# Performance work log

Hardware: AMD Instinct MI355X
Metric: run time of the kernel (lower is better)

## Reference

```python
import jax, jax.numpy as jnp
import numpy as np

B, L, K, NRBF = 2, 2048, 32, 16
NODE_F, EDGE_F = 128, 128
MAX_REL = 32  # af2 relpos -> 2*32+1 = 65 bins
NODE_IN, EDGE_IN = 21 + 6 + 8, 65 + 25 * NRBF + 1 + 2


def _ln(x, g, b, eps=1e-5):
    mu = jnp.mean(x, -1, keepdims=True)
    var = jnp.var(x, -1, keepdims=True)
    return (x - mu) / jnp.sqrt(var + eps) * g + b


def _normalize(t):
    return jnp.nan_to_num(t / jnp.linalg.norm(t, axis=-1, keepdims=True))


def _dihedral(p0, p1, p2, p3):
    u0, u1, u2 = p2 - p1, p0 - p1, p3 - p2
    n1 = _normalize(jnp.cross(u0, u1))
    n2 = _normalize(jnp.cross(u0, u2))
    sgn = jnp.sign(jnp.sum(jnp.cross(u1, u2) * u0, -1))
    return jnp.nan_to_num(sgn * jnp.arccos(jnp.sum(n1 * n2, -1)))


def setup_inputs() -> dict:
    key = jax.random.key(0)
    ks = jax.random.split(key, 9)
    return {
        "X": jax.random.normal(ks[0], (B, L, 4, 3), jnp.float32) * 5.0,
        "S": jax.random.randint(ks[1], (B, L), 0, 21),
        "BB_D_sincos": jax.random.normal(ks[2], (B, L, 3, 2), jnp.float32),
        "SC_D_sincos": jax.random.normal(ks[3], (B, L, 4, 2), jnp.float32),
        "chain_indices": jax.random.randint(ks[4], (B, L), 0, 2),
        "mask": jnp.ones((B, L), jnp.float32),
        "W_node": jax.random.normal(ks[5], (NODE_IN, NODE_F), jnp.float32) * 0.05,
        "b_node": jnp.zeros((NODE_F,), jnp.float32),
        "g_node": jnp.ones((NODE_F,), jnp.float32),
        "beta_node": jnp.zeros((NODE_F,), jnp.float32),
        "W_edge": jax.random.normal(ks[6], (EDGE_IN, EDGE_F), jnp.float32) * 0.05,
        "b_edge": jnp.zeros((EDGE_F,), jnp.float32),
        "g_edge": jnp.ones((EDGE_F,), jnp.float32),
        "beta_edge": jnp.zeros((EDGE_F,), jnp.float32),
    }


def reference(X, S, BB_D_sincos, SC_D_sincos, chain_indices, mask,
              W_node, b_node, g_node, beta_node,
              W_edge, b_edge, g_edge, beta_edge):
    Bn, Ln = X.shape[:2]
    N, Ca, C, O = X[:, :, 0], X[:, :, 1], X[:, :, 2], X[:, :, 3]
    # ---- masked pairwise Ca distances + kNN topk (smallest) ----
    m2 = mask[:, None, :] * mask[:, :, None]                      # [B,L,L]
    dX = Ca[:, :, None, :] - Ca[:, None, :, :]
    D = m2 * jnp.sqrt(jnp.sum(dX * dX, -1) + 1e-6)
    D_adj = D + 2.0 * (1.0 - m2) * jnp.max(D, -1, keepdims=True)
    _, E_idx = jax.lax.top_k(-D_adj, K)                           # [B,L,K]
    bidx = jnp.arange(Bn)[:, None, None]
    # ---- af2 relative-position one-hot (residue_index=None path) ----
    offset = E_idx - jnp.arange(Ln)[None, :, None]
    E_pos = jax.nn.one_hot(jnp.clip(offset + MAX_REL, 0, 2 * MAX_REL),
                           2 * MAX_REL + 1, dtype=jnp.float32)    # [B,L,K,65]
    # ---- impute CB, 5x5 atomic-distance RBFs at neighbors only ----
    bv, cv = Ca - N, C - Ca
    Cb = -0.58273431 * jnp.cross(bv, cv) + 0.56802827 * bv - 0.54067466 * cv + Ca
    X5 = jnp.stack((N, Ca, C, O, Cb), axis=-2)                    # [B,L,5,3]
    X5_nb = X5[bidx, E_idx]                                       # [B,L,K,5,3]
    dA = X5[:, :, None, :, None, :] - X5_nb[:, :, :, None, :, :]  # [B,L,K,5i,5j,3]
    Dn = jnp.sqrt(jnp.sum(dA * dA, -1) + 1e-6)                    # [B,L,K,5,5]
    mu = jnp.linspace(0.0, 20.0, NRBF)
    sigma = 20.0 / NRBF
    RBF_all = jnp.exp(-(((Dn[..., None] - mu) / sigma) ** 2))
    RBF_all = RBF_all.reshape(Bn, Ln, K, 25 * NRBF)               # i-major, j, rbf order
    # ---- edge type: same-chain indicator + 1 ----
    ch_nb = chain_indices[bidx, E_idx]
    E_type = ((ch_nb == chain_indices[:, :, None]).astype(jnp.float32) + 1.0)[..., None]
    # ---- pairwise dihedrals, evaluated only at neighbors ----
    N_nb, Ca_nb, C_nb = N[bidx, E_idx], Ca[bidx, E_idx], C[bidx, E_idx]
    ir_phi = _dihedral(C[:, :, None, :], N_nb, Ca_nb, C_nb)
    ir_psi = _dihedral(N[:, :, None, :], Ca[:, :, None, :], C[:, :, None, :], N_nb)
    dihed = jnp.stack((ir_phi, ir_psi), -1)                       # [B,L,K,2]
    # ---- fuse + embed ----
    E = jnp.concatenate((E_pos, RBF_all, E_type, dihed), -1)      # [B,L,K,468]
    V = jnp.concatenate((jax.nn.one_hot(S, 21, dtype=jnp.float32),
                         BB_D_sincos.reshape(Bn, Ln, -1),
                         SC_D_sincos.reshape(Bn, Ln, -1)), -1)    # [B,L,35]
    h_V = _ln(V @ W_node + b_node, g_node, beta_node)
    h_E = _ln(E @ W_edge + b_edge, g_edge, beta_edge)
    return (h_V, h_E, E_idx, X)
```

## Files before the change

kernel.cpp:

```cpp
#include <hip/hip_runtime.h>
#include <math.h>

#define NB 2
#define NL 2048
#define NK 32
#define NODE_F 128
#define EDGE_F 128

#define OFF_HV   0
#define OFF_HE   (NB*NL*NODE_F)
#define OFF_EIDX (OFF_HE + NB*NL*NK*EDGE_F)
#define OFF_X    (OFF_EIDX + NB*NL*NK)

#define ACH 7
#define BCH 6
#define SAW 232

typedef __attribute__((ext_vector_type(8))) short v8s;
typedef __attribute__((ext_vector_type(4))) float v4f;

__device__ __forceinline__ short f2bf(float f) {
    unsigned u = __float_as_uint(f);
    unsigned r = u + 0x7fffu + ((u >> 16) & 1u);
    return (short)(r >> 16);
}

#if __has_builtin(__builtin_amdgcn_exp2f)
#define EXP2F(x) __builtin_amdgcn_exp2f(x)
#else
#define EXP2F(x) __expf((x) * 0.6931471805599453f)
#endif

__device__ __forceinline__ unsigned bfpack(float f0, float f1) {
    unsigned u0 = __float_as_uint(f0), u1 = __float_as_uint(f1);
#if __has_builtin(__builtin_amdgcn_perm)
    return __builtin_amdgcn_perm(u1, u0, 0x07060302u);
#else
    return (u1 & 0xFFFF0000u) | (u0 >> 16);
#endif
}

template<int CTRL>
__device__ __forceinline__ unsigned long long dpp_min_step(unsigned long long x) {
    unsigned lo = (unsigned)x, hi = (unsigned)(x >> 32);
    unsigned plo = (unsigned)__builtin_amdgcn_update_dpp((int)lo, (int)lo, CTRL, 0xF, 0xF, false);
    unsigned phi = (unsigned)__builtin_amdgcn_update_dpp((int)hi, (int)hi, CTRL, 0xF, 0xF, false);
    unsigned long long p = (((unsigned long long)phi) << 32) | plo;
    return p < x ? p : x;
}
__device__ __forceinline__ unsigned long long wave_min_u64_dpp(unsigned long long x) {
    x = dpp_min_step<0xB1>(x);
    x = dpp_min_step<0x4E>(x);
    x = dpp_min_step<0x141>(x);
    x = dpp_min_step<0x140>(x);
    x = dpp_min_step<0x142>(x);
    x = dpp_min_step<0x143>(x);
    return x;
}

__device__ __forceinline__ void cross3(const float a[3], const float b[3], float c[3]) {
    c[0] = a[1]*b[2] - a[2]*b[1];
    c[1] = a[2]*b[0] - a[0]*b[2];
    c[2] = a[0]*b[1] - a[1]*b[0];
}
__device__ __forceinline__ float dot3(const float a[3], const float b[3]) {
    return a[0]*b[0] + a[1]*b[1] + a[2]*b[2];
}
__device__ float dihedral_f(const float p0[3], const float p1[3],
                            const float p2[3], const float p3[3]) {
    float u0[3], u1[3], u2[3];
    for (int d = 0; d < 3; d++) {
        u0[d] = p2[d] - p1[d];
        u1[d] = p0[d] - p1[d];
        u2[d] = p3[d] - p2[d];
    }
    float n1[3], n2[3], c12[3];
    cross3(u0, u1, n1);
    cross3(u0, u2, n2);
    cross3(u1, u2, c12);
    float l1 = sqrtf(dot3(n1, n1));
    float l2 = sqrtf(dot3(n2, n2));
    float cosang = dot3(n1, n2) / (l1 * l2);
    float s = dot3(c12, u0);
    float sgn = (s > 0.f) ? 1.f : ((s < 0.f) ? -1.f : 0.f);
    float r = sgn * acosf(cosang);
    return isnan(r) ? 0.f : r;
}

#define KNN_QMIN(Q) {                                                                  \
    unsigned long long a_ = key[(Q)*8+0] < key[(Q)*8+1] ? key[(Q)*8+0] : key[(Q)*8+1]; \
    unsigned long long b_ = key[(Q)*8+2] < key[(Q)*8+3] ? key[(Q)*8+2] : key[(Q)*8+3]; \
    unsigned long long c_ = key[(Q)*8+4] < key[(Q)*8+5] ? key[(Q)*8+4] : key[(Q)*8+5]; \
    unsigned long long d_ = key[(Q)*8+6] < key[(Q)*8+7] ? key[(Q)*8+6] : key[(Q)*8+7]; \
    a_ = a_ < b_ ? a_ : b_; c_ = c_ < d_ ? c_ : d_;                                    \
    qm[(Q)] = a_ < c_ ? a_ : c_; }

#define KNN_STEP(Q) {                                                                  \
    _Pragma("unroll")                                                                  \
    for (int i_ = 0; i_ < 8; i_++)                                                     \
        key[(Q)*8+i_] = (me && tstar == (Q)*8+i_) ? ~0ull : key[(Q)*8+i_];             \
    KNN_QMIN(Q) }

__global__ __launch_bounds__(256) void fused_pre_kernel(const float* __restrict__ X,
                                                        const float* __restrict__ mask,
                                                        const int* __restrict__ S,
                                                        const float* __restrict__ BB,
                                                        const float* __restrict__ SC,
                                                        const float* __restrict__ Wn,
                                                        const float* __restrict__ bn,
                                                        const float* __restrict__ gn,
                                                        const float* __restrict__ betan,
                                                        const float* __restrict__ We,
                                                        const float* __restrict__ be,
                                                        float* __restrict__ X5,
                                                        short* __restrict__ WTf,
                                                        int* __restrict__ EidxW,
                                                        float* __restrict__ out) {
    __shared__ float sCa[NL * 3];
    int blk = blockIdx.x;
    int tid = threadIdx.x;

    if (blk >= 1024) {
        if (blk < 1040) {
            int row = (blk - 1024) * 256 + tid;
            float v[12];
#pragma unroll
            for (int t = 0; t < 12; t++) v[t] = X[row * 12 + t];
#pragma unroll
            for (int t = 0; t < 12; t++) out[OFF_X + row * 12 + t] = v[t];
            float bv[3], cv[3], cr[3];
            for (int d = 0; d < 3; d++) { bv[d] = v[3+d] - v[d]; cv[d] = v[6+d] - v[3+d]; }
            cross3(bv, cv, cr);
            float* x5 = X5 + row * 15;
#pragma unroll
            for (int t = 0; t < 12; t++) x5[t] = v[t];
            for (int d = 0; d < 3; d++)
                x5[12 + d] = -0.58273431f * cr[d] + 0.56802827f * bv[d] - 0.54067466f * cv[d] + v[3+d];
        } else {
            int t = (blk - 1040) * 256 + tid;
            if (t >= 13 * 8 * 64) return;
            int lane = t & 63;
            int nt = (t >> 6) & 7;
            int ch = t >> 9;
            int n = nt * 16 + (lane & 15);
            int kbase = ch * 32 + (lane >> 4) * 8;
            short* dst = WTf + (size_t)t * 8;
#pragma unroll
            for (int j = 0; j < 8; j++) {
                int k = kbase + j;
                float f;
                if (k < 403) f = We[(65 + k) * 128 + n];
                else if (k == 403) f = be[n];
                else f = 0.f;
                dst[j] = f2bf(f);
            }
        }
        return;
    }

    int w = tid >> 6, l = tid & 63;
    int row = blk * 4 + w;
    int b = row / NL;
    int base = b * NL;

    for (int idx = tid; idx < NL; idx += 256) {
        const float* xp = X + (size_t)(base + idx) * 12 + 3;
        sCa[idx * 3 + 0] = xp[0];
        sCa[idx * 3 + 1] = xp[1];
        sCa[idx * 3 + 2] = xp[2];
    }

    {
        int f0 = l, f1 = 64 + l;
        int s = S[row];
        float a0 = bn[f0] + Wn[s * NODE_F + f0];
        float a1 = bn[f1] + Wn[s * NODE_F + f1];
#pragma unroll
        for (int t = 0; t < 6; t++) {
            float x = BB[row * 6 + t];
            a0 += x * Wn[(21 + t) * NODE_F + f0];
            a1 += x * Wn[(21 + t) * NODE_F + f1];
        }
#pragma unroll
        for (int t = 0; t < 8; t++) {
            float x = SC[row * 8 + t];
            a0 += x * Wn[(27 + t) * NODE_F + f0];
            a1 += x * Wn[(27 + t) * NODE_F + f1];
        }
        float sm = a0 + a1;
#pragma unroll
        for (int st = 1; st < 64; st <<= 1) sm += __shfl_xor(sm, st, 64);
        float mean = sm * (1.0f / 128.0f);
        float d0 = a0 - mean, d1 = a1 - mean;
        float q = d0 * d0 + d1 * d1;
#pragma unroll
        for (int st = 1; st < 64; st <<= 1) q += __shfl_xor(q, st, 64);
        float rstd = 1.0f / sqrtf(q * (1.0f / 128.0f) + 1e-5f);
        out[OFF_HV + row * NODE_F + f0] = d0 * rstd * gn[f0] + betan[f0];
        out[OFF_HV + row * NODE_F + f1] = d1 * rstd * gn[f1] + betan[f1];
    }
    __syncthreads();

    const float* mrow = mask + base;
    int lrow = row - base;
    float cx = sCa[lrow * 3 + 0], cy = sCa[lrow * 3 + 1], cz = sCa[lrow * 3 + 2];
    float mi = mrow[lrow];

    float K[32];
    float lmax = 0.0f;
#pragma unroll
    for (int t = 0; t < 32; t++) {
        int j = t * 64 + l;
        float dx = __fsub_rn(cx, sCa[j * 3 + 0]);
        float dy = __fsub_rn(cy, sCa[j * 3 + 1]);
        float dz = __fsub_rn(cz, sCa[j * 3 + 2]);
        float ss = __fadd_rn(__fadd_rn(__fadd_rn(__fmul_rn(dx, dx), __fmul_rn(dy, dy)),
                                       __fmul_rn(dz, dz)), 1e-6f);
        float d = __fmul_rn(__fmul_rn(mi, mrow[j]), __fsqrt_rn(ss));
        K[t] = d;
        lmax = fmaxf(lmax, d);
    }
#pragma unroll
    for (int s = 1; s < 64; s <<= 1) lmax = fmaxf(lmax, __shfl_xor(lmax, s, 64));
#pragma unroll
    for (int t = 0; t < 32; t++) {
        int j = t * 64 + l;
        float m2 = __fmul_rn(mi, mrow[j]);
        K[t] = __fadd_rn(K[t], __fmul_rn(__fmul_rn(2.0f, __fsub_rn(1.0f, m2)), lmax));
    }

    unsigned long long key[32];
#pragma unroll
    for (int t = 0; t < 32; t++)
        key[t] = (((unsigned long long)__float_as_uint(K[t])) << 32) | (unsigned)(t * 64 + l);

    unsigned long long qm[4];
    KNN_QMIN(0) KNN_QMIN(1) KNN_QMIN(2) KNN_QMIN(3)

    int selj = 0;
#pragma unroll 1
    for (int r = 0; r < NK; r++) {
        unsigned long long m01 = qm[0] < qm[1] ? qm[0] : qm[1];
        unsigned long long m23 = qm[2] < qm[3] ? qm[2] : qm[3];
        unsigned long long g = m01 < m23 ? m01 : m23;
        g = wave_min_u64_dpp(g);
        unsigned j = (unsigned)__builtin_amdgcn_readlane((int)(unsigned)g, 63);
        if (l == r) selj = (int)j;
        bool me = ((j & 63u) == (unsigned)l);
        int tstar = (int)(j >> 6);
        switch (tstar >> 3) {
            case 0: KNN_STEP(0) break;
            case 1: KNN_STEP(1) break;
            case 2: KNN_STEP(2) break;
            default: KNN_STEP(3) break;
        }
    }
    if (l < NK) {
        EidxW[row * NK + l] = selj;
        out[OFF_EIDX + row * NK + l] = (float)selj;
    }
}

__global__ __launch_bounds__(256, 4) void edge8_kernel(const float* __restrict__ X5,
                                                       const int* __restrict__ Eidx,
                                                       const int* __restrict__ chain,
                                                       const float* __restrict__ We,
                                                       const float* __restrict__ ge,
                                                       const float* __restrict__ betae,
                                                       const short* __restrict__ WTf,
                                                       float* __restrict__ out) {
    __shared__ short sA[64 * SAW];
    __shared__ float sXj[64][17];
    __shared__ float sXi[2][15];
    __shared__ float sRow[2][128];
    __shared__ int   sJ[64];
    __shared__ int   sPos[64];
    __shared__ float sEt[64], sPhi[64], sPsi[64];

    int tid = threadIdx.x;
    int e0 = blockIdx.x * 64;
    int b = e0 / (NL * NK);
    int i0 = (e0 / NK) % NL;
    int lane = tid & 63, w = tid >> 6;

    if (tid < 64) sJ[tid] = Eidx[e0 + tid];
    if (tid < 30) sXi[tid / 15][tid % 15] = X5[(b * NL + i0 + tid / 15) * 15 + (tid % 15)];
    if (tid >= 128 && tid < 128 + 128) {
        int n2 = tid - 128;
        sRow[0][n2] = ge[n2];
        sRow[1][n2] = betae[n2];
    }
    __syncthreads();

    for (int t = tid; t < 64 * 15; t += 256) {
        int e = t / 15, c2 = t % 15;
        sXj[e][c2] = X5[(b * NL + sJ[e]) * 15 + c2];
    }
    if (tid < 64) {
        int e = tid;
        int i = i0 + (e >> 5);
        int j = sJ[e];
        int off = j - i + 32;
        off = off < 0 ? 0 : (off > 64 ? 64 : off);
        sPos[e] = off;
        sEt[e] = (chain[b * NL + j] == chain[b * NL + i]) ? 2.0f : 1.0f;
    }
    __syncthreads();

    if (tid < 128) {
        int e = tid & 63;
        const float* xi = sXi[e >> 5];
        const float* xj = sXj[e];
        if (tid < 64) sPhi[e] = dihedral_f(&xi[6], &xj[0], &xj[3], &xj[6]);
        else          sPsi[e] = dihedral_f(&xi[0], &xi[3], &xi[6], &xj[0]);
    }

    const float Ac  = -0.92332482616893658f;
    const float K1c = 2.46219953645049755f;
    const float Rc  = EXP2F(-1.64146635763366503f);
    const float R2c = Rc * Rc;
    int eg_ = w * 16 + (lane & 15);
    int q_ = lane >> 4;
    const float* xiG = sXi[eg_ >> 5];
    const float* xjG = sXj[eg_];
    short* rowp = sA + eg_ * SAW;
    float hfq = (float)(q_ & 1);

#define GEN_A(hh, CNT)                                                         \
    {                                                                          \
        _Pragma("unroll")                                                      \
        for (int t = 0; t < (CNT); t++) {                                      \
            int o = q_ + t * 4;                                                \
            int kg = (hh) * 224 + o * 8;                                       \
            int pair = kg >> 4;                                                \
            union { unsigned u[4]; v8s v; } au;                                \
            if (pair >= 25) {                                                  \
                if ((hh) == 1 && o == 22) {         \
                    au.u[0] = bfpack(sEt[eg_], sPhi[eg_]);                     \
                    au.u[1] = bfpack(sPsi[eg_], 1.0f);                         \
                    au.u[2] = 0; au.u[3] = 0;                                  \
                } else {                                                       \
                    au.u[0] = 0; au.u[1] = 0; au.u[2] = 0; au.u[3] = 0;        \
                }                                                              \
            } else {                                                           \
                int a = pair / 5, cc = pair - a * 5;                           \
                float dx = xiG[a*3+0] - xjG[cc*3+0];                           \
                float dy = xiG[a*3+1] - xjG[cc*3+1];                           \
                float dz = xiG[a*3+2] - xjG[cc*3+2];                           \
                float d = sqrtf(dx*dx + dy*dy + dz*dz + 1e-6f);                \
                float ee = fminf(__fmaf_rn(hfq, -10.666666666666666f, d), 40.f); \
                float r0 = EXP2F(Ac * ee * ee);                                \
                float g  = EXP2F(K1c * ee) * Rc;                               \
                float r1 = r0 * g; g *= R2c;                                   \
                float r2 = r1 * g; g *= R2c;                                   \
                float r3 = r2 * g; g *= R2c;                                   \
                float r4 = r3 * g; g *= R2c;                                   \
                float r5 = r4 * g; g *= R2c;                                   \
                float r6 = r5 * g; g *= R2c;                                   \
                float r7 = r6 * g;                                             \
                au.u[0] = bfpack(r0, r1);                                      \
                au.u[1] = bfpack(r2, r3);                                      \
                au.u[2] = bfpack(r4, r5);                                      \
                au.u[3] = bfpack(r6, r7);                                      \
            }                                                                  \
            *(v8s*)(rowp + o * 8) = au.v;                                      \
        }                                                                      \
    }

    GEN_A(0, ACH)
    __syncthreads();

    int cl = lane & 15, kq = lane >> 4;
    int ntA = 2 * w, ntB = ntA + 1;
    const char* sAc = (const char*)sA;
    int abase0 = cl * (SAW * 2) + kq * 16;

    v4f acc[4][2];
#pragma unroll
    for (int eg = 0; eg < 4; eg++) { acc[eg][0] = (v4f){0.f,0.f,0.f,0.f}; acc[eg][1] = (v4f){0.f,0.f,0.f,0.f}; }

#define MMA_HALF(CHBASE, CNT)                                                  \
    {                                                                          \
        _Pragma("unroll 2")                                                    \
        for (int chl = 0; chl < (CNT); chl++) {                                \
            const v8s* gb = (const v8s*)WTf + ((size_t)((CHBASE) + chl) * 512 + lane); \
            v8s b0 = gb[ntA * 64];                                             \
            v8s b1 = gb[ntB * 64];                                             \
            int ab = abase0 + chl * 64;                                        \
            v8s a0 = *(const v8s*)(sAc + ab);                                  \
            v8s a1 = *(const v8s*)(sAc + ab + 16 * (SAW * 2));                 \
            v8s a2 = *(const v8s*)(sAc + ab + 32 * (SAW * 2));                 \
            v8s a3 = *(const v8s*)(sAc + ab + 48 * (SAW * 2));                 \
            acc[0][0] = __builtin_amdgcn_mfma_f32_16x16x32_bf16(a0, b0, acc[0][0], 0, 0, 0); \
            acc[0][1] = __builtin_amdgcn_mfma_f32_16x16x32_bf16(a0, b1, acc[0][1], 0, 0, 0); \
            acc[1][0] = __builtin_amdgcn_mfma_f32_16x16x32_bf16(a1, b0, acc[1][0], 0, 0, 0); \
            acc[1][1] = __builtin_amdgcn_mfma_f32_16x16x32_bf16(a1, b1, acc[1][1], 0, 0, 0); \
            acc[2][0] = __builtin_amdgcn_mfma_f32_16x16x32_bf16(a2, b0, acc[2][0], 0, 0, 0); \
            acc[2][1] = __builtin_amdgcn_mfma_f32_16x16x32_bf16(a2, b1, acc[2][1], 0, 0, 0); \
            acc[3][0] = __builtin_amdgcn_mfma_f32_16x16x32_bf16(a3, b0, acc[3][0], 0, 0, 0); \
            acc[3][1] = __builtin_amdgcn_mfma_f32_16x16x32_bf16(a3, b1, acc[3][1], 0, 0, 0); \
        }                                                                      \
    }

    MMA_HALF(0, ACH)
    __syncthreads();
    GEN_A(1, BCH)
    __syncthreads();
    MMA_HALF(ACH, BCH)

    float2* sRed = (float2*)&sXj[0][0];
    int nA = ntA * 16 + cl, nB = nA + 16;
    float r4A = sRow[0][nA], r5A = sRow[1][nA];
    float r4B = sRow[0][nB], r5B = sRow[1][nB];

#pragma unroll
    for (int eg = 0; eg < 4; eg++) {
#pragma unroll
        for (int r = 0; r < 4; r++) {
            int e = eg * 16 + kq * 4 + r;
            int pos = sPos[e];
            float v0 = acc[eg][0][r] + We[pos * 128 + nA];
            float v1 = acc[eg][1][r] + We[pos * 128 + nB];
            acc[eg][0][r] = v0; acc[eg][1][r] = v1;
            float s = v0 + v1, q2 = v0 * v0 + v1 * v1;
#pragma unroll
            for (int s2 = 1; s2 < 16; s2 <<= 1) {
                s  += __shfl_xor(s,  s2, 64);
                q2 += __shfl_xor(q2, s2, 64);
            }
            if (cl == 0) sRed[e * 4 + w] = make_float2(s, q2);
        }
    }
    __syncthreads();

#pragma unroll
    for (int eg = 0; eg < 4; eg++) {
#pragma unroll
        for (int r = 0; r < 4; r++) {
            int e = eg * 16 + kq * 4 + r;
            float4 pa = *(const float4*)&sRed[e * 4];
            float4 pb = *(const float4*)&sRed[e * 4 + 2];
            float s  = pa.x + pa.z + pb.x + pb.z;
            float q2 = pa.y + pa.w + pb.y + pb.w;
            float mean = s * (1.0f / 128.0f);
            float var = q2 * (1.0f / 128.0f) - mean * mean;
            float rstd = rsqrtf(var + 1e-5f);
            size_t base = OFF_HE + (size_t)(e0 + e) * 128;
            out[base + nA] = (acc[eg][0][r] - mean) * rstd * r4A + r5A;
            out[base + nB] = (acc[eg][1][r] - mean) * rstd * r4B + r5B;
        }
    }
}

extern "C" void kernel_launch(void* const* d_in, const int* in_sizes, int n_in,
                              void* d_out, int out_size, void* d_ws, size_t ws_size,
                              hipStream_t stream) {
    (void)in_sizes; (void)n_in; (void)out_size; (void)ws_size;
    const float* X    = (const float*)d_in[0];
    const int*   S    = (const int*)d_in[1];
    const float* BB   = (const float*)d_in[2];
    const float* SC   = (const float*)d_in[3];
    const int*   chain= (const int*)d_in[4];
    const float* mask = (const float*)d_in[5];
    const float* Wn   = (const float*)d_in[6];
    const float* bn   = (const float*)d_in[7];
    const float* gn   = (const float*)d_in[8];
    const float* betan= (const float*)d_in[9];
    const float* We   = (const float*)d_in[10];
    const float* be   = (const float*)d_in[11];
    const float* ge   = (const float*)d_in[12];
    const float* betae= (const float*)d_in[13];
    float* out = (float*)d_out;

    char* ws = (char*)d_ws;
    int*   EidxW = (int*)ws;
    float* X5    = (float*)(ws + 524288);
    short* WTf   = (short*)(ws + 770048);

    hipLaunchKernelGGL(fused_pre_kernel, dim3(1024 + 16 + 26), dim3(256), 0, stream,
                       X, mask, S, BB, SC, Wn, bn, gn, betan, We, be,
                       X5, WTf, EidxW, out);
    hipLaunchKernelGGL(edge8_kernel, dim3(NB * NL * NK / 64), dim3(256), 0, stream,
                       X5, EidxW, chain, We, ge, betae, WTf, out);
}
```

Measured before the change: 182.0 us.

## Replace kNN top-k loop with threshold binary search and compacted candidate selection

The per-row k-nearest-neighbour selection no longer runs 32 rounds of 64-bit wave-wide minimum over 32 keys per lane. Instead it binary-searches a float-bit threshold with ballot/popcount until between 32 and 64 candidates fall under it. Those candidates are compacted into shared memory at one per lane, and 32 rounds of a cheaper 32-bit DPP min plus ballot pick the winners. This cuts per-round register work and 64-bit shuffles, but adds up to 31 search iterations of 32 ballots each. It also relies on the compaction order to keep the original tie-breaking by index.

```diff
diff --git a/kernel.cpp b/kernel.cpp
--- a/kernel.cpp
+++ b/kernel.cpp
@@ -41,20 +41,17 @@
 }
 
 template<int CTRL>
-__device__ __forceinline__ unsigned long long dpp_min_step(unsigned long long x) {
-    unsigned lo = (unsigned)x, hi = (unsigned)(x >> 32);
-    unsigned plo = (unsigned)__builtin_amdgcn_update_dpp((int)lo, (int)lo, CTRL, 0xF, 0xF, false);
-    unsigned phi = (unsigned)__builtin_amdgcn_update_dpp((int)hi, (int)hi, CTRL, 0xF, 0xF, false);
-    unsigned long long p = (((unsigned long long)phi) << 32) | plo;
+__device__ __forceinline__ unsigned dpp_min_u32_step(unsigned x) {
+    unsigned p = (unsigned)__builtin_amdgcn_update_dpp((int)x, (int)x, CTRL, 0xF, 0xF, false);
     return p < x ? p : x;
 }
-__device__ __forceinline__ unsigned long long wave_min_u64_dpp(unsigned long long x) {
-    x = dpp_min_step<0xB1>(x);
-    x = dpp_min_step<0x4E>(x);
-    x = dpp_min_step<0x141>(x);
-    x = dpp_min_step<0x140>(x);
-    x = dpp_min_step<0x142>(x);
-    x = dpp_min_step<0x143>(x);
+__device__ __forceinline__ unsigned wave_min_u32_dpp(unsigned x) {
+    x = dpp_min_u32_step<0xB1>(x);
+    x = dpp_min_u32_step<0x4E>(x);
+    x = dpp_min_u32_step<0x141>(x);
+    x = dpp_min_u32_step<0x140>(x);
+    x = dpp_min_u32_step<0x142>(x);
+    x = dpp_min_u32_step<0x143>(x);
     return x;
 }
 
@@ -86,20 +83,6 @@
     float r = sgn * acosf(cosang);
     return isnan(r) ? 0.f : r;
 }
-
-#define KNN_QMIN(Q) {                                                                  \
-    unsigned long long a_ = key[(Q)*8+0] < key[(Q)*8+1] ? key[(Q)*8+0] : key[(Q)*8+1]; \
-    unsigned long long b_ = key[(Q)*8+2] < key[(Q)*8+3] ? key[(Q)*8+2] : key[(Q)*8+3]; \
-    unsigned long long c_ = key[(Q)*8+4] < key[(Q)*8+5] ? key[(Q)*8+4] : key[(Q)*8+5]; \
-    unsigned long long d_ = key[(Q)*8+6] < key[(Q)*8+7] ? key[(Q)*8+6] : key[(Q)*8+7]; \
-    a_ = a_ < b_ ? a_ : b_; c_ = c_ < d_ ? c_ : d_;                                    \
-    qm[(Q)] = a_ < c_ ? a_ : c_; }
-
-#define KNN_STEP(Q) {                                                                  \
-    _Pragma("unroll")                                                                  \
-    for (int i_ = 0; i_ < 8; i_++)                                                     \
-        key[(Q)*8+i_] = (me && tstar == (Q)*8+i_) ? ~0ull : key[(Q)*8+i_];             \
-    KNN_QMIN(Q) }
 
 __global__ __launch_bounds__(256) void fused_pre_kernel(const float* __restrict__ X,
                                                         const float* __restrict__ mask,
@@ -117,6 +100,7 @@
                                                         int* __restrict__ EidxW,
                                                         float* __restrict__ out) {
     __shared__ float sCa[NL * 3];
+    __shared__ unsigned long long sSel[4][64];
     int blk = blockIdx.x;
     int tid = threadIdx.x;
 
@@ -229,31 +213,48 @@
         K[t] = __fadd_rn(K[t], __fmul_rn(__fmul_rn(2.0f, __fsub_rn(1.0f, m2)), lmax));
     }
 
-    unsigned long long key[32];
-#pragma unroll
-    for (int t = 0; t < 32; t++)
-        key[t] = (((unsigned long long)__float_as_uint(K[t])) << 32) | (unsigned)(t * 64 + l);
-
-    unsigned long long qm[4];
-    KNN_QMIN(0) KNN_QMIN(1) KNN_QMIN(2) KNN_QMIN(3)
-
+    unsigned lo_ = 0u, hi_ = 0x7f7fffffu, tau = 0x7f7fffffu;
+#pragma unroll 1
+    for (int it = 0; it < 31; it++) {
+        unsigned mid = (lo_ + hi_) >> 1;
+        float tf = __uint_as_float(mid);
+        int c = 0;
+#pragma unroll
+        for (int t = 0; t < 32; t++) c += __popcll(__ballot(K[t] <= tf));
+        if (c >= 32) {
+            tau = mid;
+            if (c <= 64) break;
+            hi_ = mid - 1;
+        } else {
+            lo_ = mid + 1;
+        }
+    }
+    float tauf = __uint_as_float(tau);
+
+    sSel[w][l] = ~0ull;
+    int cbase = 0;
+#pragma unroll
+    for (int t = 0; t < 32; t++) {
+        bool q = (K[t] <= tauf);
+        unsigned long long m = __ballot(q);
+        int pos = cbase + __popcll(m & ((1ull << l) - 1ull));
+        if (q && pos < 64)
+            sSel[w][pos] = (((unsigned long long)__float_as_uint(K[t])) << 32)
+                           | (unsigned)(t * 64 + l);
+        cbase += __popcll(m);
+    }
+
+    unsigned long long key = sSel[w][l];
     int selj = 0;
 #pragma unroll 1
     for (int r = 0; r < NK; r++) {
-        unsigned long long m01 = qm[0] < qm[1] ? qm[0] : qm[1];
-        unsigned long long m23 = qm[2] < qm[3] ? qm[2] : qm[3];
-        unsigned long long g = m01 < m23 ? m01 : m23;
-        g = wave_min_u64_dpp(g);
-        unsigned j = (unsigned)__builtin_amdgcn_readlane((int)(unsigned)g, 63);
+        unsigned hi = (unsigned)(key >> 32);
+        unsigned gh = (unsigned)__builtin_amdgcn_readlane((int)wave_min_u32_dpp(hi), 63);
+        unsigned long long mask_ = __ballot(hi == gh);
+        int wl = __ffsll((unsigned long long)mask_) - 1;
+        unsigned j = (unsigned)__builtin_amdgcn_readlane((int)(unsigned)key, wl);
         if (l == r) selj = (int)j;
-        bool me = ((j & 63u) == (unsigned)l);
-        int tstar = (int)(j >> 6);
-        switch (tstar >> 3) {
-            case 0: KNN_STEP(0) break;
-            case 1: KNN_STEP(1) break;
-            case 2: KNN_STEP(2) break;
-            default: KNN_STEP(3) break;
-        }
+        if (l == wl) key = ~0ull;
     }
     if (l < NK) {
         EidxW[row * NK + l] = selj;
```

Measured after the change: 159.6 us. 1.14x faster.
